# Performance work log

Hardware: AMD Instinct MI355X
Metric: run time of the kernel (lower is better)

## Reference

```python
import jax, jax.numpy as jnp
import numpy as np

OUT, IN = 4096, 4096
BLOCK = 32
NBLK = IN // BLOCK  # 128


def setup_inputs() -> dict:
    key = jax.random.key(0)
    k1, k2, k3 = jax.random.split(key, 3)
    x = jax.random.normal(k1, (2, 2048, IN), dtype=jnp.float32)
    # per-block scales (GGUF stores fp16 scales; small magnitude typical)
    scales = jax.random.normal(k2, (OUT, NBLK), dtype=jnp.float32) * 0.01
    # int8 codes stored as unsigned 0..255; signed value = code - 128
    codes = jax.random.randint(k3, (OUT, NBLK, BLOCK), 0, 256, dtype=jnp.int32)
    return {"x": x, "scales": scales, "codes": codes}


def dequantize_q8_0(scales, codes):
    # scales: [out, nblk], codes: [out, nblk, 32] unsigned -> signed int8 semantics
    signed = codes.astype(jnp.float32) - 128.0
    w = scales[:, :, None] * signed            # [out, nblk, 32]
    return w.reshape(OUT, IN)                   # [out, in]


def reference(x, scales, codes):
    weight = dequantize_q8_0(scales, codes)     # [out, in]
    # nn.functional.linear: y = x @ weight.T
    return jnp.einsum("bsi,oi->bso", x, weight)
```

## Files before the change

### kernel.cpp

```cpp
#include <hip/hip_runtime.h>
#include <hip/hip_bf16.h>
#include <stdint.h>


#define M_DIM 4096
#define N_DIM 4096
#define K_DIM 4096
#define TILE 128
#define BK 64

typedef __attribute__((ext_vector_type(8))) short bf16x8;
typedef __attribute__((ext_vector_type(4))) float f32x4;

__device__ __forceinline__ unsigned short f32_to_bf16_rne(float f) {
    unsigned u = __float_as_uint(f);
    u += 0x7fffu + ((u >> 16) & 1u);
    return (unsigned short)(u >> 16);
}

__device__ __forceinline__ void load_lds16(const void* g, void* l) {
    __builtin_amdgcn_global_load_lds(
        (const __attribute__((address_space(1))) unsigned int*)g,
        (__attribute__((address_space(3))) unsigned int*)l, 16, 0, 0);
}

__global__ __launch_bounds__(256) void prologue_kernel(
        const int* __restrict__ codes, const float* __restrict__ scales,
        unsigned short* __restrict__ W,
        const float* __restrict__ x, unsigned short* __restrict__ xb) {
    const int bid = blockIdx.x;
    if (bid < 16384) {
        const int tid = bid * 256 + threadIdx.x;
        const float s = scales[(tid >> 10) * 128 + ((tid >> 3) & 127)];
        const int4 c = ((const int4*)codes)[tid];
        union { unsigned short u[4]; uint2 v; } p;
        p.u[0] = f32_to_bf16_rne(s * (float)(c.x - 128));
        p.u[1] = f32_to_bf16_rne(s * (float)(c.y - 128));
        p.u[2] = f32_to_bf16_rne(s * (float)(c.z - 128));
        p.u[3] = f32_to_bf16_rne(s * (float)(c.w - 128));
        ((uint2*)W)[tid] = p.v;
    } else {
        const int tid = (bid - 16384) * 256 + threadIdx.x;
        const float4 f = ((const float4*)x)[tid];
        union { unsigned short u[4]; uint2 v; } p;
        p.u[0] = f32_to_bf16_rne(f.x); p.u[1] = f32_to_bf16_rne(f.y);
        p.u[2] = f32_to_bf16_rne(f.z); p.u[3] = f32_to_bf16_rne(f.w);
        ((uint2*)xb)[tid] = p.v;
    }
}

__global__ __launch_bounds__(256) void gemm_bt_kernel(
        const unsigned short* __restrict__ A,
        const unsigned short* __restrict__ B,
        float* __restrict__ C) {
    __shared__ unsigned short As[TILE * BK];
    __shared__ unsigned short Bs[TILE * BK];

    const int wave = threadIdx.x >> 6;
    const int lane = threadIdx.x & 63;

    const int b   = blockIdx.x;
    const int i   = b >> 3;
    const int mt0 = ((b >> 2) & 1) * 16 + (i & 15);
    const int nt0 = (b & 3) * 8 + (i >> 4);
    const int m0 = mt0 * TILE;
    const int n0 = nt0 * TILE;

    const int srow  = lane >> 3;
    const int skofs = ((lane & 7) ^ srow) * 8;
    const int wrow0 = wave * 32;

    const unsigned short* Ag = A + (size_t)(m0 + wrow0 + srow) * K_DIM + skofs;
    const unsigned short* Bg = B + (size_t)(n0 + wrow0 + srow) * K_DIM + skofs;
    unsigned short* AsBase = &As[wrow0 * BK];
    unsigned short* BsBase = &Bs[wrow0 * BK];

    const int frow = lane & 15;
    const int quad = lane >> 4;
    const int wm = (wave >> 1) * 64;
    const int wn = (wave & 1) * 64;

    f32x4 acc[4][4] = {};

    for (int k0 = 0; k0 < K_DIM; k0 += BK) {
#pragma unroll
        for (int j = 0; j < 4; ++j) {
            load_lds16(Ag + k0 + j * 8 * K_DIM, AsBase + j * 8 * BK);
            load_lds16(Bg + k0 + j * 8 * K_DIM, BsBase + j * 8 * BK);
        }
        __syncthreads();

#pragma unroll
        for (int h = 0; h < 2; ++h) {
            bf16x8 a[4], bfr[4];
#pragma unroll
            for (int t = 0; t < 4; ++t) {
                const int ar = wm + t * 16 + frow;
                const int br = wn + t * 16 + frow;
                const int ch = (h * 4 + quad) ^ (frow & 7);
                a[t]   = *(const bf16x8*)&As[ar * BK + ch * 8];
                bfr[t] = *(const bf16x8*)&Bs[br * BK + ch * 8];
            }
#pragma unroll
            for (int mt = 0; mt < 4; ++mt)
#pragma unroll
                for (int nt = 0; nt < 4; ++nt)
                    acc[mt][nt] = __builtin_amdgcn_mfma_f32_16x16x32_bf16(
                        a[mt], bfr[nt], acc[mt][nt], 0, 0, 0);
        }
        __syncthreads();
    }

#pragma unroll
    for (int mt = 0; mt < 4; ++mt)
#pragma unroll
        for (int nt = 0; nt < 4; ++nt)
#pragma unroll
            for (int r = 0; r < 4; ++r) {
                const int row = m0 + wm + mt * 16 + quad * 4 + r;
                const int col = n0 + wn + nt * 16 + frow;
                C[(size_t)row * N_DIM + col] = acc[mt][nt][r];
            }
}

extern "C" void kernel_launch(void* const* d_in, const int* in_sizes, int n_in,
                              void* d_out, int out_size, void* d_ws, size_t ws_size,
                              hipStream_t stream) {
    const float* x      = (const float*)d_in[0];
    const float* scales = (const float*)d_in[1];
    const int*   codes  = (const int*)d_in[2];
    float* y = (float*)d_out;

    unsigned short* Wb = (unsigned short*)d_ws;
    unsigned short* xb = (unsigned short*)((char*)d_ws + (size_t)N_DIM * K_DIM * 2);

    prologue_kernel<<<32768, 256, 0, stream>>>(codes, scales, Wb, x, xb);

    gemm_bt_kernel<<<1024, 256, 0, stream>>>(xb, Wb, y);
}
```

Before: 321.6 us.

## Load B fragments directly from global into registers, bypassing LDS

The GEMM stops staging the weight tile in LDS: each wave loads its B MFMA fragments straight from global memory into registers, and only A goes through LDS. This halves LDS usage and drops the B LDS reads, and a launch-bounds occupancy hint of 4 is added. The swizzled block ordering is replaced by a plain 2D grid. The risk is that B rows are now fetched by both waves sharing an N half, with no LDS reuse, which doubles global/L2 traffic for B. The loads are exposed latency before the barrier, and L2 locality from the old tile remapping is lost.

```diff
diff --git a/kernel.cpp b/kernel.cpp
--- a/kernel.cpp
+++ b/kernel.cpp
@@ -49,64 +49,62 @@
     }
 }
 
-__global__ __launch_bounds__(256) void gemm_bt_kernel(
+__global__ __launch_bounds__(256, 4) void gemm_bt_kernel(
         const unsigned short* __restrict__ A,
         const unsigned short* __restrict__ B,
         float* __restrict__ C) {
     __shared__ unsigned short As[TILE * BK];
-    __shared__ unsigned short Bs[TILE * BK];
 
     const int wave = threadIdx.x >> 6;
     const int lane = threadIdx.x & 63;
 
-    const int b   = blockIdx.x;
-    const int i   = b >> 3;
-    const int mt0 = ((b >> 2) & 1) * 16 + (i & 15);
-    const int nt0 = (b & 3) * 8 + (i >> 4);
-    const int m0 = mt0 * TILE;
-    const int n0 = nt0 * TILE;
+    const int m0 = blockIdx.y * TILE;
+    const int n0 = blockIdx.x * TILE;
 
     const int srow  = lane >> 3;
     const int skofs = ((lane & 7) ^ srow) * 8;
     const int wrow0 = wave * 32;
 
     const unsigned short* Ag = A + (size_t)(m0 + wrow0 + srow) * K_DIM + skofs;
-    const unsigned short* Bg = B + (size_t)(n0 + wrow0 + srow) * K_DIM + skofs;
     unsigned short* AsBase = &As[wrow0 * BK];
-    unsigned short* BsBase = &Bs[wrow0 * BK];
 
     const int frow = lane & 15;
     const int quad = lane >> 4;
     const int wm = (wave >> 1) * 64;
     const int wn = (wave & 1) * 64;
 
+    const unsigned short* Bg = B + (size_t)(n0 + wn + frow) * K_DIM + quad * 8;
+
     f32x4 acc[4][4] = {};
 
     for (int k0 = 0; k0 < K_DIM; k0 += BK) {
 #pragma unroll
-        for (int j = 0; j < 4; ++j) {
+        for (int j = 0; j < 4; ++j)
             load_lds16(Ag + k0 + j * 8 * K_DIM, AsBase + j * 8 * BK);
-            load_lds16(Bg + k0 + j * 8 * K_DIM, BsBase + j * 8 * BK);
-        }
+
+        bf16x8 b[2][4];
+#pragma unroll
+        for (int h = 0; h < 2; ++h)
+#pragma unroll
+            for (int t = 0; t < 4; ++t)
+                b[h][t] = *(const bf16x8*)(Bg + (size_t)t * 16 * K_DIM
+                                              + k0 + h * 32);
         __syncthreads();
 
 #pragma unroll
         for (int h = 0; h < 2; ++h) {
-            bf16x8 a[4], bfr[4];
+            bf16x8 a[4];
 #pragma unroll
             for (int t = 0; t < 4; ++t) {
-                const int ar = wm + t * 16 + frow;
-                const int br = wn + t * 16 + frow;
                 const int ch = (h * 4 + quad) ^ (frow & 7);
-                a[t]   = *(const bf16x8*)&As[ar * BK + ch * 8];
-                bfr[t] = *(const bf16x8*)&Bs[br * BK + ch * 8];
+                a[t] = *(const bf16x8*)&As[(wm + t * 16 + frow) * BK + ch * 8];
             }
 #pragma unroll
             for (int mt = 0; mt < 4; ++mt)
 #pragma unroll
                 for (int nt = 0; nt < 4; ++nt)
                     acc[mt][nt] = __builtin_amdgcn_mfma_f32_16x16x32_bf16(
-                        a[mt], bfr[nt], acc[mt][nt], 0, 0, 0);
+                        a[mt], b[h][nt], acc[mt][nt], 0, 0, 0);
         }
         __syncthreads();
     }
@@ -136,5 +134,6 @@
 
     prologue_kernel<<<32768, 256, 0, stream>>>(codes, scales, Wb, x, xb);
 
-    gemm_bt_kernel<<<1024, 256, 0, stream>>>(xb, Wb, y);
+    dim3 grid(N_DIM / TILE, M_DIM / TILE);
+    gemm_bt_kernel<<<grid, 256, 0, stream>>>(xb, Wb, y);
 }
```

New measurement: 536.5 us. 66.8% more time.
